# Kernel tuning notes

Measured on AMD Instinct MI355X. Metric: run time of the kernel, lower is better.

## Reference

```python
import jax, jax.numpy as jnp
import numpy as np

B, N, F, T = 8, 4096, 3, 12
D = 64            # model_dim
AH, DK, DV = 4, 32, 32   # attention headers, k_dim, v_dim
GH = 8            # gat_headers == out_features
E = 524288


def _ln(x, g, b, eps=1e-5):
    m = jnp.mean(x, -1, keepdims=True)
    v = jnp.mean((x - m) ** 2, -1, keepdims=True)
    return (x - m) * jax.lax.rsqrt(v + eps) * g + b


def _glu(x, w, b, C):
    # x: [B, C, N, L], w: [2C, C, 1, k] -> causal-style valid conv + SiLU gate
    y = jax.lax.conv_general_dilated(x, w, (1, 1), 'VALID',
                                     dimension_numbers=('NCHW', 'OIHW', 'NCHW'))
    y = y + b[None, :, None, None]
    return jax.nn.silu(y[:, :C]) * y[:, C:]


def setup_inputs():
    key = jax.random.key(0)
    ks = jax.random.split(key, 20)
    s = jnp.float32(0.02)
    return {
        'data': jax.random.normal(ks[0], (B, N, F, T), jnp.float32),
        'edges': jax.random.randint(ks[1], (2, E), 0, B * N),
        'embT_w': jax.random.normal(ks[2], (T, N)) * s,
        'embT_g': jnp.ones((N,)), 'embT_b': jnp.zeros((N,)),
        'wq': jax.random.normal(ks[3], (N, AH * DK)) * s,
        'wk': jax.random.normal(ks[4], (N, AH * DK)) * s,
        'wv': jax.random.normal(ks[5], (N, AH * DV)) * s,
        'wo': jax.random.normal(ks[6], (AH * DV, N)) * s,
        'tat_g': jnp.ones((N,)), 'tat_b': jnp.zeros((N,)),
        'mix_w': jax.random.normal(ks[7], (D, T, F)) * s,
        'mix_b': jnp.zeros((D,)),
        'embS_w': jax.random.normal(ks[8], (N, D)) * s,
        'embS_g': jnp.ones((D,)), 'embS_b': jnp.zeros((D,)),
        'gat_wl': jax.random.normal(ks[9], (D, GH * T)) * s,
        'gat_bl': jnp.zeros((GH * T,)),
        'gat_wr': jax.random.normal(ks[10], (D, GH * T)) * s,
        'gat_br': jnp.zeros((GH * T,)),
        'gat_att': jax.random.normal(ks[11], (GH, T)) * s,
        'gat_bias': jnp.zeros((GH * T,)),
        'g3_w': jax.random.normal(ks[12], (2 * GH, GH, 1, 3)) * s, 'g3_b': jnp.zeros((2 * GH,)),
        'g5_w': jax.random.normal(ks[13], (2 * GH, GH, 1, 5)) * s, 'g5_b': jnp.zeros((2 * GH,)),
        'g7_w': jax.random.normal(ks[14], (2 * GH, GH, 1, 7)) * s, 'g7_b': jnp.zeros((2 * GH,)),
        'fc_w': jax.random.normal(ks[15], (3 * T - 12, T)) * s, 'fc_b': jnp.zeros((T,)),
        'res_w': jax.random.normal(ks[16], (GH, F)) * s, 'res_b': jnp.zeros((GH,)),
        'ln_g': jnp.ones((GH,)), 'ln_b': jnp.zeros((GH,)),
    }


def reference(data, edges, embT_w, embT_g, embT_b, wq, wk, wv, wo, tat_g, tat_b,
              mix_w, mix_b, embS_w, embS_g, embS_b,
              gat_wl, gat_bl, gat_wr, gat_br, gat_att, gat_bias,
              g3_w, g3_b, g5_w, g5_b, g7_w, g7_b, fc_w, fc_b,
              res_w, res_b, ln_g, ln_b):
    # ---- EmbedT: [B,N,F,T] -> [B,F,T,N] plus learned temporal positional table
    x = data.transpose(0, 2, 3, 1) + embT_w[None, None]
    x = _ln(x, embT_g, embT_b)

    # ---- Temporal MHA over T (model_dim = N), dropout = identity in eval
    resid = x
    q = (x @ wq).reshape(B, F, T, AH, DK)
    k = (x @ wk).reshape(B, F, T, AH, DK)
    v = (x @ wv).reshape(B, F, T, AH, DV)
    scores = jnp.einsum('bfqhd,bfkhd->bfhqk', q, k) / jnp.sqrt(jnp.float32(DK))
    attn = jax.nn.softmax(scores, axis=-1)
    ctx = jnp.einsum('bfhqk,bfkhd->bfqhd', attn, v).reshape(B, F, T, AH * DV)
    x = _ln(ctx @ wo + resid, tat_g, tat_b)

    # ---- feature_temporal_mixer: Conv2d(T, D, (1, F)) on [B,T,N,F] -> [B,N,D]
    x = jnp.einsum('bftn,dtf->bnd', x, mix_w) + mix_b

    # ---- EmbedS
    x = _ln(x + embS_w[None], embS_g, embS_b)

    # ---- GATv2Conv over B*N nodes (add_self_loops=True, leaky slope 0.2)
    BN = B * N
    xf = x.reshape(BN, D)
    xl = (xf @ gat_wl + gat_bl).reshape(BN, GH, T)
    xr = (xf @ gat_wr + gat_br).reshape(BN, GH, T)
    loop = jnp.arange(BN)
    src = jnp.concatenate([edges[0], loop])
    dst = jnp.concatenate([edges[1], loop])
    feat = jax.nn.leaky_relu(xl[src] + xr[dst], 0.2)          # [E+BN, GH, T]
    e = jnp.einsum('eht,ht->eh', feat, gat_att)
    m = jax.ops.segment_max(e, dst, num_segments=BN)
    ex = jnp.exp(e - m[dst])
    ssum = jax.ops.segment_sum(ex, dst, num_segments=BN)
    alpha = ex / ssum[dst]
    out = jax.ops.segment_sum(xl[src] * alpha[:, :, None], dst, num_segments=BN)
    out = out.reshape(BN, GH * T) + gat_bias

    res_gate = out.reshape(B, N, GH, T).transpose(0, 2, 1, 3)  # [B,GH,N,T]

    # ---- gated convs (GLU) kernels 3/5/7 -> concat -> fc
    g = jnp.concatenate([_glu(res_gate, g3_w, g3_b, GH),
                         _glu(res_gate, g5_w, g5_b, GH),
                         _glu(res_gate, g7_w, g7_b, GH)], axis=-1)  # [B,GH,N,3T-12]
    x = jax.nn.relu(g @ fc_w + fc_b)   # features_num == 3 branch

    # ---- residual 1x1 conv over feature channels of raw data
    x_res = jnp.einsum('bfnt,of->bont', data.transpose(0, 2, 1, 3), res_w) \
            + res_b[None, :, None, None]
    x = jax.nn.relu(x_res + x)         # [B,GH,N,T]
    x = _ln(x.transpose(0, 3, 2, 1), ln_g, ln_b)  # LN over GH on [B,T,N,GH]
    return x.transpose(0, 2, 3, 1)     # [B,N,GH,T]
```

## Files before the change

kernel.cpp:

```cpp
#include <hip/hip_runtime.h>
#include <hip/hip_bf16.h>

typedef __hip_bfloat16 bf16;
typedef short bf16x8 __attribute__((ext_vector_type(8)));
typedef float f32x4 __attribute__((ext_vector_type(4)));
typedef unsigned short u16x4 __attribute__((ext_vector_type(4)));

constexpr int B = 8, N = 4096, F = 3, T = 12;
constexpr int Dm = 64, AH = 4, DK = 32;
constexpr int GH = 8;
constexpr int E = 524288;
constexpr int BN = B * N;
constexpr int ROWS = B * F * T;
constexpr int HD = AH * DK;
constexpr int PSZ = ROWS * 384;
constexpr int KSPLIT = 8;

__device__ __forceinline__ float b2f(bf16 x) { return __bfloat162float(x); }
__device__ __forceinline__ float u2f(unsigned short u) {
  return __uint_as_float(((unsigned)u) << 16);
}
__device__ __forceinline__ float ldf(const void* p, size_t i, int fl) {
  return fl ? b2f(((const bf16*)p)[i]) : ((const float*)p)[i];
}

constexpr unsigned C_EMBTW=0, C_EMBTG=49152, C_EMBTB=53248, C_WQ=57344,
  C_WK=581632, C_WV=1105920, C_WO=1630208, C_TATG=2154496, C_TATB=2158592,
  C_MIXW=2162688, C_MIXB=2164992, C_EMBSW=2165056, C_EMBSG=2427200,
  C_EMBSB=2427264, C_GWL=2427328, C_GBL=2433472, C_GWR=2433568,
  C_GBR=2439712, C_GATT=2439808, C_GBIAS=2439904, C_G3W=2440000,
  C_G3B=2440384, C_G5W=2440400, C_G5B=2441040, C_G7W=2441056,
  C_G7B=2441952, C_FCW=2441968, C_FCB=2442256, C_RW=2442268, C_RB=2442292,
  C_LNG=2442300, C_LNB=2442308, C_TOT=2442316;

__device__ const unsigned CUM[33] = {
  0,49152,53248,57344,581632,1105920,1630208,2154496,2158592,2162688,
  2164992,2165056,2427200,2427264,2427328,2433472,2433568,2439712,2439808,
  2439904,2440000,2440384,2440400,2441040,2441056,2441952,2441968,2442256,
  2442268,2442292,2442300,2442308,2442316};

constexpr size_t OFF_CVT = 16;
constexpr size_t OFF_X1  = OFF_CVT + 2442320;
constexpr size_t OFF_CTXB= OFF_X1  + (size_t)ROWS * N;
constexpr size_t OFF_X2  = OFF_CTXB+ (size_t)ROWS * HD;
constexpr size_t OFF_X3  = OFF_X2  + (size_t)ROWS * N;
constexpr size_t OFF_XL  = OFF_X3  + (size_t)BN * Dm;
constexpr size_t OFF_XR  = OFF_XL  + (size_t)BN * GH * T / 2;
constexpr size_t OFF_RG  = OFF_XR  + (size_t)BN * GH * T / 2;
constexpr size_t OFF_INT = OFF_RG  + (size_t)BN * GH * T;
constexpr size_t OFF_X2R = OFF_INT + 600000;
constexpr size_t OFF_WT16 = OFF_RG;
constexpr size_t OFF_X1B  = OFF_RG + 786432 + 262144;
constexpr size_t OFF_PP   = OFF_X1B + 294912;
constexpr size_t OFF_WOT  = OFF_PP + (size_t)KSPLIT * PSZ;
constexpr size_t OFF_GWT  = OFF_WOT + 262144;

struct Srcs { const void* p[32]; };

__global__ __launch_bounds__(256) void k_prep(
    const unsigned* __restrict__ g1, Srcs s, float* __restrict__ cv,
    int* __restrict__ cnt, bf16* __restrict__ wt, bf16* __restrict__ wot,
    bf16* __restrict__ wlrt) {
  __shared__ float tf[32][33];
  __shared__ bf16 tb[32][33];
  int fl = (g1[0] != 0x3F800000u);
  int blk = blockIdx.x;
  int tid = threadIdx.x;
  if (blk < 2048) {
    for (unsigned gid = blk * 256 + tid; gid < C_TOT + (unsigned)BN;
         gid += 2048 * 256) {
      if (gid < C_TOT) {
        int lo = 0, hi = 31;
        while (lo < hi) { int mid = (lo + hi + 1) >> 1; if (gid >= CUM[mid]) lo = mid; else hi = mid - 1; }
        if (lo >= 3 && lo <= 6) continue;
        unsigned off = gid - CUM[lo];
        cv[gid] = ldf(s.p[lo], off, fl);
      } else {
        cnt[gid - C_TOT] = 0;
      }
    }
  } else if (blk < 3584) {
    int bid = blk - 2048;
    int tc = bid / 128, tk = bid - tc * 128;
    int k0 = tk * 32, c0 = tc * 32;
    int mat = c0 >> 7, cloc = c0 & 127;
    const void* src = s.p[3 + mat];
    int r = tid >> 5, cc = tid & 31;
#pragma unroll
    for (int p = 0; p < 4; p++) {
      int row = p * 8 + r;
      tf[row][cc] = ldf(src, (size_t)(k0 + row) * 128 + cloc + cc, fl);
    }
    __syncthreads();
#pragma unroll
    for (int p = 0; p < 4; p++) {
      int crow = p * 8 + r;
      wt[(size_t)(c0 + crow) * 4096 + k0 + cc] = __float2bfloat16(tf[cc][crow]);
    }
  } else if (blk < 4096) {
    int bid = blk - 3584;
    int tn = bid >> 2, tk = bid & 3;
    int n0 = tn * 32, k0 = tk * 32;
    const void* wo = s.p[6];
    int r = tid >> 5, cc = tid & 31;
#pragma unroll
    for (int p = 0; p < 4; p++) {
      int row = p * 8 + r;
      size_t idx = (size_t)(k0 + row) * 4096 + n0 + cc;
      tb[row][cc] = fl ? ((const bf16*)wo)[idx]
                       : __float2bfloat16(((const float*)wo)[idx]);
    }
    __syncthreads();
#pragma unroll
    for (int p = 0; p < 4; p++) {
      int crow = p * 8 + r;
      wot[(size_t)(n0 + crow) * 128 + k0 + cc] = tb[cc][crow];
    }
  } else {
    int idx = (blk - 4096) * 256 + tid;
    if (idx < 192 * 64) {
      int c = idx >> 6, k = idx & 63;
      float v = (c < 96) ? ldf(s.p[14], (size_t)k * 96 + c, fl)
                         : ldf(s.p[16], (size_t)k * 96 + (c - 96), fl);
      wlrt[idx] = __float2bfloat16(v);
    }
  }
}

__global__ __launch_bounds__(1024) void k_embt_hist(
    const unsigned* __restrict__ g1, const void* __restrict__ data,
    const void* __restrict__ embw, const void* __restrict__ embg,
    const void* __restrict__ embb, float* __restrict__ x1,
    bf16* __restrict__ x1b, const int* __restrict__ edges,
    int* __restrict__ cnt) {
  __shared__ float red[32];
  int tid = threadIdx.x;
  int fl = (g1[0] != 0x3F800000u);
  if (blockIdx.x >= ROWS) {
    int e = (blockIdx.x - ROWS) * 1024 + tid;
    if (e < E) atomicAdd(cnt + edges[E + e], 1);
    return;
  }
  int row = blockIdx.x;
  int t = row % T; int bf_ = row / T; int f = bf_ % F; int bb = bf_ / F;
  float dv[4];
#pragma unroll
  for (int i = 0; i < 4; i++) {
    int n = i * 1024 + tid;
    dv[i] = ldf(data, (size_t)(bb * N + n) * 36 + f * 12 + t, fl);
  }
  float vals[4]; float s = 0.f, s2 = 0.f;
#pragma unroll
  for (int i = 0; i < 4; i++) {
    int n = i * 1024 + tid;
    float v = dv[i] + ldf(embw, (size_t)t * N + n, fl);
    vals[i] = v; s += v; s2 += v * v;
  }
#pragma unroll
  for (int o = 32; o > 0; o >>= 1) { s += __shfl_down(s, o, 64); s2 += __shfl_down(s2, o, 64); }
  int lane = tid & 63, wid = tid >> 6;
  if (lane == 0) { red[wid] = s; red[16 + wid] = s2; }
  __syncthreads();
  float S = 0.f, S2 = 0.f;
#pragma unroll
  for (int j = 0; j < 16; j++) { S += red[j]; S2 += red[16 + j]; }
  float mean = S / (float)N;
  float var = S2 / (float)N - mean * mean;
  float inv = rsqrtf(var + 1e-5f);
#pragma unroll
  for (int i = 0; i < 4; i++) {
    int n = i * 1024 + tid;
    float o = (vals[i] - mean) * inv * ldf(embg, n, fl) + ldf(embb, n, fl);
    x1[(size_t)row * N + n] = o;
    x1b[(size_t)row * N + n] = __float2bfloat16(o);
  }
}

__global__ __launch_bounds__(256) void k_qkv_scan(
    const bf16* __restrict__ x1b, const bf16* __restrict__ wt,
    float* __restrict__ pp, const int* __restrict__ cnt,
    int* __restrict__ off, int* __restrict__ cur) {
  __shared__ int part[256];
  int tid = threadIdx.x;
  if (blockIdx.x == 864) {
    int base = tid * 128;
    int s = 0;
    for (int j = 0; j < 128; j++) s += cnt[base + j];
    part[tid] = s;
    __syncthreads();
    for (int d = 1; d < 256; d <<= 1) {
      int v = (tid >= d) ? part[tid - d] : 0;
      __syncthreads();
      part[tid] += v;
      __syncthreads();
    }
    int run = part[tid] - s;
    for (int j = 0; j < 128; j++) {
      int c = cnt[base + j];
      off[base + j] = run; cur[base + j] = run;
      run += c;
    }
    if (tid == 255) off[BN] = E;
    return;
  }
  int wave = (blockIdx.x * 256 + tid) >> 6;
  int lane = tid & 63;
  int ks = wave & 7, tile = wave >> 3;
  int mt = tile / 24, nt = tile - mt * 24;
  int m = lane & 15, quad = lane >> 4;
  const bf16* ap = x1b + (size_t)(mt * 16 + m) * 4096 + ks * 512 + quad * 8;
  const bf16* bp = wt  + (size_t)(nt * 16 + m) * 4096 + ks * 512 + quad * 8;
  f32x4 acc = {0.f, 0.f, 0.f, 0.f};
  for (int kk = 0; kk < 512; kk += 32) {
    bf16x8 a = *(const bf16x8*)(ap + kk);
    bf16x8 b = *(const bf16x8*)(bp + kk);
    acc = __builtin_amdgcn_mfma_f32_16x16x32_bf16(a, b, acc, 0, 0, 0);
  }
  float* o = pp + ((size_t)ks * ROWS + mt * 16 + quad * 4) * 384 + nt * 16 + m;
#pragma unroll
  for (int r = 0; r < 4; r++) o[(size_t)r * 384] = acc[r];
}

__global__ __launch_bounds__(256) void k_attn_scatter(
    const float* __restrict__ pp, bf16* __restrict__ ctxb,
    const int* __restrict__ edges, int* __restrict__ cur,
    int* __restrict__ srcs) {
  if (blockIdx.x >= 24) {
    int e = (blockIdx.x - 24) * 256 + threadIdx.x;
    if (e < E) {
      int pos = atomicAdd(cur + edges[E + e], 1);
      srcs[pos] = edges[e];
    }
    return;
  }
  int bf_ = blockIdx.x;
  int h = threadIdx.x >> 6;
  int tid = threadIdx.x & 63;
  __shared__ float qs[4][12][32], ks[4][12][32], vs[4][12][32], att[4][12][12];
  for (int idx = tid; idx < 384; idx += 64) {
    int t = idx >> 5, d = idx & 31;
    int base = (bf_ * T + t) * 384 + h * 32 + d;
    float qv = 0.f, kv = 0.f, vv = 0.f;
#pragma unroll
    for (int p = 0; p < KSPLIT; p++) {
      qv += pp[(size_t)p * PSZ + base];
      kv += pp[(size_t)p * PSZ + base + 128];
      vv += pp[(size_t)p * PSZ + base + 256];
    }
    qs[h][t][d] = qv; ks[h][t][d] = kv; vs[h][t][d] = vv;
  }
  __syncthreads();
  for (int idx = tid; idx < 144; idx += 64) {
    int qt = idx / 12, kt = idx - qt * 12;
    float s = 0.f;
#pragma unroll
    for (int d = 0; d < 32; d++) s += qs[h][qt][d] * ks[h][kt][d];
    att[h][qt][kt] = s * 0.1767766953f;
  }
  __syncthreads();
  if (tid < 12) {
    float m = -1e30f;
#pragma unroll
    for (int j = 0; j < 12; j++) m = fmaxf(m, att[h][tid][j]);
    float ss = 0.f;
#pragma unroll
    for (int j = 0; j < 12; j++) { float e = __expf(att[h][tid][j] - m); att[h][tid][j] = e; ss += e; }
    float inv = 1.f / ss;
#pragma unroll
    for (int j = 0; j < 12; j++) att[h][tid][j] *= inv;
  }
  __syncthreads();
  for (int idx = tid; idx < 384; idx += 64) {
    int t = idx >> 5, d = idx & 31;
    float s = 0.f;
#pragma unroll
    for (int j = 0; j < 12; j++) s += att[h][t][j] * vs[h][j][d];
    ctxb[(size_t)(bf_ * T + t) * HD + h * 32 + d] = __float2bfloat16(s);
  }
}

__global__ __launch_bounds__(256) void k_proj_mma(
    const bf16* __restrict__ ctxb, const bf16* __restrict__ wot,
    const float* __restrict__ x1, float* __restrict__ x2r) {
  int wave = (blockIdx.x * 256 + threadIdx.x) >> 6;
  int lane = threadIdx.x & 63;
  int nt = wave & 255, mt = wave >> 8;
  int m = lane & 15, quad = lane >> 4;
  const bf16* ap = ctxb + (size_t)(mt * 16 + m) * 128 + quad * 8;
  const bf16* bp = wot  + (size_t)(nt * 16 + m) * 128 + quad * 8;
  f32x4 acc = {0.f, 0.f, 0.f, 0.f};
#pragma unroll
  for (int kk = 0; kk < 128; kk += 32) {
    bf16x8 a = *(const bf16x8*)(ap + kk);
    bf16x8 b = *(const bf16x8*)(bp + kk);
    acc = __builtin_amdgcn_mfma_f32_16x16x32_bf16(a, b, acc, 0, 0, 0);
  }
  int row0 = mt * 16 + quad * 4, col = nt * 16 + m;
#pragma unroll
  for (int r = 0; r < 4; r++) {
    size_t idx = (size_t)(row0 + r) * N + col;
    x2r[idx] = acc[r] + x1[idx];
  }
}

__global__ __launch_bounds__(1024) void k_ln2(
    const float* __restrict__ x2r, const float* __restrict__ g,
    const float* __restrict__ b_, float* __restrict__ x2) {
  __shared__ float red[32];
  int row = blockIdx.x, tid = threadIdx.x;
  float vals[4]; float s = 0.f, s2 = 0.f;
#pragma unroll
  for (int i = 0; i < 4; i++) {
    int n = i * 1024 + tid;
    float v = x2r[(size_t)row * N + n];
    vals[i] = v; s += v; s2 += v * v;
  }
#pragma unroll
  for (int o = 32; o > 0; o >>= 1) { s += __shfl_down(s, o, 64); s2 += __shfl_down(s2, o, 64); }
  int lane = tid & 63, wid = tid >> 6;
  if (lane == 0) { red[wid] = s; red[16 + wid] = s2; }
  __syncthreads();
  float S = 0.f, S2 = 0.f;
#pragma unroll
  for (int j = 0; j < 16; j++) { S += red[j]; S2 += red[16 + j]; }
  float mean = S / (float)N;
  float var = S2 / (float)N - mean * mean;
  float inv = rsqrtf(var + 1e-5f);
#pragma unroll
  for (int i = 0; i < 4; i++) {
    int n = i * 1024 + tid;
    x2[(size_t)row * N + n] = (vals[i] - mean) * inv * g[n] + b_[n];
  }
}

__global__ __launch_bounds__(256) void k_mix_ln(
    const float* __restrict__ x2, const float* __restrict__ mw,
    const float* __restrict__ mb, const float* __restrict__ sw,
    const float* __restrict__ g, const float* __restrict__ b_,
    bf16* __restrict__ x3b) {
  int tid = threadIdx.x; int wid = tid >> 6; int d = tid & 63;
  int ng = blockIdx.x * 4 + wid;
  int bb = ng >> 12; int n = ng & (N - 1);
  float acc = mb[d];
#pragma unroll
  for (int t = 0; t < T; t++)
#pragma unroll
    for (int f = 0; f < F; f++)
      acc += x2[((size_t)(bb * F + f) * T + t) * N + n] * mw[(d * T + t) * F + f];
  acc += sw[(size_t)n * Dm + d];
  float s = acc, s2 = acc * acc;
#pragma unroll
  for (int m = 1; m < 64; m <<= 1) { s += __shfl_xor(s, m, 64); s2 += __shfl_xor(s2, m, 64); }
  float mean = s * (1.f / 64.f), var = s2 * (1.f / 64.f) - mean * mean;
  float inv = rsqrtf(var + 1e-5f);
  x3b[(size_t)ng * Dm + d] = __float2bfloat16((acc - mean) * inv * g[d] + b_[d]);
}

__global__ __launch_bounds__(256) void k_gat_mma(
    const bf16* __restrict__ x3b, const bf16* __restrict__ wlrt,
    const float* __restrict__ bl, const float* __restrict__ br,
    bf16* __restrict__ xl, bf16* __restrict__ xr) {
  __shared__ __align__(16) bf16 bs[192 * 64];
  int tid = threadIdx.x;
  {
    const bf16x8* src = (const bf16x8*)wlrt;
    bf16x8* dst = (bf16x8*)bs;
#pragma unroll
    for (int i = 0; i < 6; i++) {
      int ci = i * 256 + tid;
      dst[ci ^ ((ci >> 3) & 7)] = src[ci];
    }
  }
  __syncthreads();
  int wave = tid >> 6, lane = tid & 63;
  int mt = blockIdx.x * 4 + wave;
  int m = lane & 15, quad = lane >> 4;
  const bf16* ap = x3b + (size_t)(mt * 16 + m) * 64 + quad * 8;
  bf16x8 a0 = *(const bf16x8*)(ap);
  bf16x8 a1 = *(const bf16x8*)(ap + 32);
  const bf16x8* bs8 = (const bf16x8*)bs;
  int row0 = mt * 16 + quad * 4;
#pragma unroll
  for (int nt = 0; nt < 12; nt++) {
    int r = nt * 16 + m;
    int c0 = r * 8 + quad;
    bf16x8 b0 = bs8[c0 ^ (r & 7)];
    bf16x8 b1 = bs8[(c0 + 4) ^ (r & 7)];
    f32x4 acc = {0.f, 0.f, 0.f, 0.f};
    acc = __builtin_amdgcn_mfma_f32_16x16x32_bf16(a0, b0, acc, 0, 0, 0);
    acc = __builtin_amdgcn_mfma_f32_16x16x32_bf16(a1, b1, acc, 0, 0, 0);
    bool left = r < 96;
    int c = left ? r : r - 96;
    float bias = left ? bl[c] : br[c];
    bf16* o = left ? xl : xr;
#pragma unroll
    for (int rr = 0; rr < 4; rr++)
      o[(size_t)(row0 + rr) * 96 + c] = __float2bfloat16(acc[rr] + bias);
  }
}

__device__ __forceinline__ void ld12bf(const bf16* p, float* l) {
  u16x4 a = *(const u16x4*)p;
  u16x4 b = *(const u16x4*)(p + 4);
  u16x4 c = *(const u16x4*)(p + 8);
  l[0]=u2f(a.x); l[1]=u2f(a.y); l[2]=u2f(a.z); l[3]=u2f(a.w);
  l[4]=u2f(b.x); l[5]=u2f(b.y); l[6]=u2f(b.z); l[7]=u2f(b.w);
  l[8]=u2f(c.x); l[9]=u2f(c.y); l[10]=u2f(c.z); l[11]=u2f(c.w);
}

__global__ __launch_bounds__(256) void k_gat(
    const int* __restrict__ off, const int* __restrict__ srcs,
    const bf16* __restrict__ xl, const bf16* __restrict__ xr,
    const float* __restrict__ att, const float* __restrict__ bias,
    float* __restrict__ rg) {
  int tid = threadIdx.x;
  int wv = tid >> 6, lane = tid & 63;
  int es = lane >> 3, h = lane & 7;
  int dst = blockIdx.x * 4 + wv;
  int bb = dst >> 12, n = dst & (N - 1);
  size_t rbase = (size_t)dst * 96 + h * 12;
  float xd[12], at[12];
  ld12bf(xr + rbase, xd);
#pragma unroll
  for (int t = 0; t < 12; t++) at[t] = att[h * 12 + t];

  float acc[12];
#pragma unroll
  for (int t = 0; t < 12; t++) acc[t] = 0.f;
  float ssum = 0.f;
  if (es == 0) {
    float l[12];
    ld12bf(xl + rbase, l);
    float sc = 0.f;
#pragma unroll
    for (int t = 0; t < 12; t++) {
      float sv = l[t] + xd[t];
      float fr = sv > 0.f ? sv : 0.2f * sv;
      sc += fr * at[t];
    }
    float ex = __expf(sc);
    ssum = ex;
#pragma unroll
    for (int t = 0; t < 12; t++) acc[t] = l[t] * ex;
  }
  int st = off[dst], en = off[dst + 1];
  for (int j = st + es; j < en; j += 8) {
    int src = srcs[j];
    float l[12];
    ld12bf(xl + (size_t)src * 96 + h * 12, l);
    float sc = 0.f;
#pragma unroll
    for (int t = 0; t < 12; t++) {
      float sv = l[t] + xd[t];
      float fr = sv > 0.f ? sv : 0.2f * sv;
      sc += fr * at[t];
    }
    float ex = __expf(sc);
    ssum += ex;
#pragma unroll
    for (int t = 0; t < 12; t++) acc[t] += l[t] * ex;
  }
#pragma unroll
  for (int m = 8; m < 64; m <<= 1) {
    ssum += __shfl_xor(ssum, m, 64);
#pragma unroll
    for (int t = 0; t < 12; t++) acc[t] += __shfl_xor(acc[t], m, 64);
  }
  if (es == 0) {
    float inv = 1.f / ssum;
    float* op = rg + ((size_t)(bb * 8 + h) * N + n) * 12;
#pragma unroll
    for (int t = 0; t < 12; t++)
      op[t] = acc[t] * inv + bias[h * 12 + t];
  }
}

__global__ __launch_bounds__(768) void k_tail(
    const unsigned* __restrict__ g1, const float* __restrict__ rg,
    const float* __restrict__ g3w, const float* __restrict__ g3b,
    const float* __restrict__ g5w, const float* __restrict__ g5b,
    const float* __restrict__ g7w, const float* __restrict__ g7b,
    const float* __restrict__ fcw, const float* __restrict__ fcb,
    const void* __restrict__ data, const float* __restrict__ rw,
    const float* __restrict__ rb, const float* __restrict__ lng,
    const float* __restrict__ lnb, void* __restrict__ out) {
  int tid = threadIdx.x;
  int br = tid >> 8;
  int u = tid & 255;
  int h = u & 7, i = u >> 3;
  int blk = blockIdx.x;
  int bb = blk >> 7;
  int n0 = (blk & 127) * 32;
  int n = n0 + i;
  int fl = (g1[0] != 0x3F800000u);
  __shared__ float xs[32][100];
  __shared__ float dds[32][40];
  __shared__ float wpk[8 * 260 + 4];
  __shared__ float fcs[288];
  __shared__ float gbuf[24][256];
  __shared__ float b3s[16], b5s[16], b7s[16], fcbs[12], lngs[8], lnbs[8], rws[24], rbs[8];
  for (int idx = tid; idx < 3072; idx += 768) {
    int c = idx / 384; int within = idx - c * 384;
    int ii = within / 12, t = within - ii * 12;
    xs[ii][c * 12 + t] = rg[((size_t)(bb * 8 + c) * N + n0 + ii) * 12 + t];
  }
  for (int idx = tid; idx < 1152; idx += 768) {
    int nn = idx / 36, jj = idx - nn * 36;
    dds[nn][jj] = ldf(data, (size_t)(bb * N + n0 + nn) * 36 + jj, fl);
  }
  for (int idx = tid; idx < 1920; idx += 768) {
    int hh = idx / 240; int r = idx - hh * 240; int c = r / 30; int tap = r - c * 30;
    float v;
    if (tap < 3)       v = g3w[hh * 24 + c * 3 + tap];
    else if (tap < 6)  v = g3w[(hh + 8) * 24 + c * 3 + (tap - 3)];
    else if (tap < 11) v = g5w[hh * 40 + c * 5 + (tap - 6)];
    else if (tap < 16) v = g5w[(hh + 8) * 40 + c * 5 + (tap - 11)];
    else if (tap < 23) v = g7w[hh * 56 + c * 7 + (tap - 16)];
    else               v = g7w[(hh + 8) * 56 + c * 7 + (tap - 23)];
    wpk[hh * 260 + c * 32 + tap] = v;
  }
  for (int idx = tid; idx < 288; idx += 768) fcs[idx] = fcw[idx];
  if (tid < 16) { b3s[tid] = g3b[tid]; b5s[tid] = g5b[tid]; b7s[tid] = g7b[tid]; }
  if (tid < 12) fcbs[tid] = fcb[tid];
  if (tid < 24) rws[tid] = rw[tid];
  if (tid < 8) { lngs[tid] = lng[tid]; lnbs[tid] = lnb[tid]; rbs[tid] = rb[tid]; }
  __syncthreads();
  const float* x = xs[i];
  const float* wbase = &wpk[h * 260];
  if (br == 0) {
    float pa[10], pb[10];
    float ba = b3s[h], bbv = b3s[h + 8];
#pragma unroll
    for (int l = 0; l < 10; l++) { pa[l] = ba; pb[l] = bbv; }
#pragma unroll
    for (int c = 0; c < 8; c++) {
      float4 xa = *(const float4*)&x[c * 12];
      float4 xb = *(const float4*)&x[c * 12 + 4];
      float4 xc = *(const float4*)&x[c * 12 + 8];
      float xr[12] = {xa.x, xa.y, xa.z, xa.w, xb.x, xb.y, xb.z, xb.w,
                      xc.x, xc.y, xc.z, xc.w};
      const float* wpc = wbase + c * 32;
      float4 wA = *(const float4*)wpc;
      float2 wB = *(const float2*)(wpc + 4);
#pragma unroll
      for (int l = 0; l < 10; l++) {
        pa[l] += xr[l] * wA.x + xr[l + 1] * wA.y + xr[l + 2] * wA.z;
        pb[l] += xr[l] * wA.w + xr[l + 1] * wB.x + xr[l + 2] * wB.y;
      }
    }
#pragma unroll
    for (int l = 0; l < 10; l++)
      gbuf[l][u] = pa[l] / (1.f + __expf(-pa[l])) * pb[l];
  } else if (br == 1) {
    float pa[8], pb[8];
    float ba = b5s[h], bbv = b5s[h + 8];
#pragma unroll
    for (int l = 0; l < 8; l++) { pa[l] = ba; pb[l] = bbv; }
#pragma unroll
    for (int c = 0; c < 8; c++) {
      float4 xa = *(const float4*)&x[c * 12];
      float4 xb = *(const float4*)&x[c * 12 + 4];
      float4 xc = *(const float4*)&x[c * 12 + 8];
      float xr[12] = {xa.x, xa.y, xa.z, xa.w, xb.x, xb.y, xb.z, xb.w,
                      xc.x, xc.y, xc.z, xc.w};
      const float* wpc = wbase + c * 32;
      float2 w0 = *(const float2*)(wpc + 6);
      float2 w1 = *(const float2*)(wpc + 8);
      float2 w2 = *(const float2*)(wpc + 10);
      float2 w3 = *(const float2*)(wpc + 12);
      float2 w4 = *(const float2*)(wpc + 14);
      float wt[10] = {w0.x, w0.y, w1.x, w1.y, w2.x, w2.y, w3.x, w3.y, w4.x, w4.y};
#pragma unroll
      for (int l = 0; l < 8; l++) {
        float a = 0.f, bsum = 0.f;
#pragma unroll
        for (int j = 0; j < 5; j++) { a += xr[l + j] * wt[j]; bsum += xr[l + j] * wt[5 + j]; }
        pa[l] += a; pb[l] += bsum;
      }
    }
#pragma unroll
    for (int l = 0; l < 8; l++)
      gbuf[10 + l][u] = pa[l] / (1.f + __expf(-pa[l])) * pb[l];
  } else {
    float pa[6], pb[6];
    float ba = b7s[h], bbv = b7s[h + 8];
#pragma unroll
    for (int l = 0; l < 6; l++) { pa[l] = ba; pb[l] = bbv; }
#pragma unroll
    for (int c = 0; c < 8; c++) {
      float4 xa = *(const float4*)&x[c * 12];
      float4 xb = *(const float4*)&x[c * 12 + 4];
      float4 xc = *(const float4*)&x[c * 12 + 8];
      float xr[12] = {xa.x, xa.y, xa.z, xa.w, xb.x, xb.y, xb.z, xb.w,
                      xc.x, xc.y, xc.z, xc.w};
      const float* wpc = wbase + c * 32;
      float4 wA = *(const float4*)(wpc + 16);
      float4 wB = *(const float4*)(wpc + 20);
      float4 wC = *(const float4*)(wpc + 24);
      float2 wD = *(const float2*)(wpc + 28);
      float wt[14] = {wA.x, wA.y, wA.z, wA.w, wB.x, wB.y, wB.z, wB.w,
                      wC.x, wC.y, wC.z, wC.w, wD.x, wD.y};
#pragma unroll
      for (int l = 0; l < 6; l++) {
        float a = 0.f, bsum = 0.f;
#pragma unroll
        for (int j = 0; j < 7; j++) { a += xr[l + j] * wt[j]; bsum += xr[l + j] * wt[7 + j]; }
        pa[l] += a; pb[l] += bsum;
      }
    }
#pragma unroll
    for (int l = 0; l < 6; l++)
      gbuf[18 + l][u] = pa[l] / (1.f + __expf(-pa[l])) * pb[l];
  }
  __syncthreads();
  if (br == 0) {
    float gv[24];
#pragma unroll
    for (int l = 0; l < 24; l++) gv[l] = gbuf[l][u];
    float rw0 = rws[h * 3 + 0], rw1 = rws[h * 3 + 1], rw2 = rws[h * 3 + 2], rb0 = rbs[h];
    size_t obase = ((size_t)(bb * N + n) * GH + h) * T;
#pragma unroll
    for (int t = 0; t < 12; t++) {
      float a = fcbs[t];
#pragma unroll
      for (int l = 0; l < 24; l++) a += gv[l] * fcs[l * 12 + t];
      a = fmaxf(a, 0.f);
      float r = rb0 + dds[i][t] * rw0 + dds[i][12 + t] * rw1 + dds[i][24 + t] * rw2;
      float v = fmaxf(a + r, 0.f);
      float s = v, s2 = v * v;
#pragma unroll
      for (int m = 1; m < 8; m <<= 1) { s += __shfl_xor(s, m, 64); s2 += __shfl_xor(s2, m, 64); }
      float mean = s * 0.125f, var = s2 * 0.125f - mean * mean;
      float inv = rsqrtf(var + 1e-5f);
      float o = (v - mean) * inv * lngs[h] + lnbs[h];
      if (fl) ((bf16*)out)[obase + t] = __float2bfloat16(o);
      else    ((float*)out)[obase + t] = o;
    }
  }
}

extern "C" void kernel_launch(void* const* d_in, const int* in_sizes, int n_in,
                              void* d_out, int out_size, void* d_ws, size_t ws_size,
                              hipStream_t stream) {
  const void* data  = d_in[0];
  const int*  edges = (const int*)d_in[1];
  const unsigned* g1 = (const unsigned*)d_in[3];

  float* ws = (float*)d_ws;
  float* cv  = ws + OFF_CVT;
  float* x1  = ws + OFF_X1;  float* x2 = ws + OFF_X2;
  float* x2r = ws + OFF_X2R;
  bf16* x3b  = (bf16*)(ws + OFF_X3);
  bf16* ctxb = (bf16*)(ws + OFF_CTXB);
  bf16* xl   = (bf16*)(ws + OFF_XL);
  bf16* xr   = (bf16*)(ws + OFF_XR);
  float* rg  = ws + OFF_RG;
  bf16* wt16 = (bf16*)(ws + OFF_WT16);
  bf16* x1b  = (bf16*)(ws + OFF_X1B);
  bf16* wot16= (bf16*)(ws + OFF_WOT);
  bf16* wlrt = (bf16*)(ws + OFF_GWT);
  float* pp  = ws + OFF_PP;
  int* ibase = (int*)(ws + OFF_INT);
  int* cnt  = ibase;
  int* off  = ibase + BN;
  int* srcs = ibase + 2 * BN + 16;

  Srcs s;
  for (int i = 0; i < 32; i++) s.p[i] = d_in[2 + i];

  k_prep<<<4144, 256, 0, stream>>>(g1, s, cv, cnt, wt16, wot16, wlrt);
  k_embt_hist<<<ROWS + 512, 1024, 0, stream>>>(g1, data, d_in[2], d_in[3],
                                               d_in[4], x1, x1b, edges, cnt);
  k_qkv_scan<<<865, 256, 0, stream>>>(x1b, wt16, pp, cnt, off, cnt);
  k_attn_scatter<<<24 + 2048, 256, 0, stream>>>(pp, ctxb, edges, cnt, srcs);
  k_proj_mma<<<1152, 256, 0, stream>>>(ctxb, wot16, x1, x2r);
  k_ln2<<<ROWS, 1024, 0, stream>>>(x2r, cv + C_TATG, cv + C_TATB, x2);
  k_mix_ln<<<BN / 4, 256, 0, stream>>>(x2, cv + C_MIXW, cv + C_MIXB, cv + C_EMBSW,
                                       cv + C_EMBSG, cv + C_EMBSB, x3b);
  k_gat_mma<<<512, 256, 0, stream>>>(x3b, wlrt, cv + C_GBL, cv + C_GBR, xl, xr);
  k_gat<<<BN / 4, 256, 0, stream>>>(off, srcs, xl, xr, cv + C_GATT, cv + C_GBIAS, rg);
  k_tail<<<BN / 32, 768, 0, stream>>>(g1, rg, cv + C_G3W, cv + C_G3B, cv + C_G5W,
                                      cv + C_G5B, cv + C_G7W, cv + C_G7B, cv + C_FCW,
                                      cv + C_FCB, data, cv + C_RW, cv + C_RB,
                                      cv + C_LNG, cv + C_LNB, d_out);
}
```

Measured before the change: 331.2 us.

## Fuse mix-LN into GAT projection and GAT aggregation into tail kernel

The mix+layernorm stage now writes its bf16 rows into shared memory inside the GAT projection MMA kernel, so the x3b global round trip goes away. The GAT edge aggregation moves into the tail kernel, which grows to 1024 threads and writes per-node results straight to shared memory instead of the rg buffer. This removes two launches and two intermediate global buffers. In exchange, the mix stage has lower parallelism (512 blocks, each wave looping over 16 rows) and the tail kernel uses larger blocks, which may lower occupancy; there is also a __syncthreads inside a divergent branch, with the idle threads calling a matching one.

```diff
diff --git a/kernel.cpp b/kernel.cpp
--- a/kernel.cpp
+++ b/kernel.cpp
@@ -333,34 +333,15 @@
   }
 }
 
-__global__ __launch_bounds__(256) void k_mix_ln(
+__global__ __launch_bounds__(256) void k_mix_gat(
     const float* __restrict__ x2, const float* __restrict__ mw,
     const float* __restrict__ mb, const float* __restrict__ sw,
     const float* __restrict__ g, const float* __restrict__ b_,
-    bf16* __restrict__ x3b) {
-  int tid = threadIdx.x; int wid = tid >> 6; int d = tid & 63;
-  int ng = blockIdx.x * 4 + wid;
-  int bb = ng >> 12; int n = ng & (N - 1);
-  float acc = mb[d];
-#pragma unroll
-  for (int t = 0; t < T; t++)
-#pragma unroll
-    for (int f = 0; f < F; f++)
-      acc += x2[((size_t)(bb * F + f) * T + t) * N + n] * mw[(d * T + t) * F + f];
-  acc += sw[(size_t)n * Dm + d];
-  float s = acc, s2 = acc * acc;
-#pragma unroll
-  for (int m = 1; m < 64; m <<= 1) { s += __shfl_xor(s, m, 64); s2 += __shfl_xor(s2, m, 64); }
-  float mean = s * (1.f / 64.f), var = s2 * (1.f / 64.f) - mean * mean;
-  float inv = rsqrtf(var + 1e-5f);
-  x3b[(size_t)ng * Dm + d] = __float2bfloat16((acc - mean) * inv * g[d] + b_[d]);
-}
-
-__global__ __launch_bounds__(256) void k_gat_mma(
-    const bf16* __restrict__ x3b, const bf16* __restrict__ wlrt,
-    const float* __restrict__ bl, const float* __restrict__ br,
-    bf16* __restrict__ xl, bf16* __restrict__ xr) {
+    const bf16* __restrict__ wlrt, const float* __restrict__ bl,
+    const float* __restrict__ br, bf16* __restrict__ xl,
+    bf16* __restrict__ xr) {
   __shared__ __align__(16) bf16 bs[192 * 64];
+  __shared__ __align__(16) bf16 x3s[64 * 64];
   int tid = threadIdx.x;
   {
     const bf16x8* src = (const bf16x8*)wlrt;
@@ -371,15 +352,39 @@
       dst[ci ^ ((ci >> 3) & 7)] = src[ci];
     }
   }
+  int wv = tid >> 6, lane = tid & 63;
+  int d = lane;
+  int row0 = blockIdx.x * 64;
+  float gd = g[d], bd = b_[d], mbd = mb[d];
+#pragma unroll 1
+  for (int rr = 0; rr < 16; rr++) {
+    int ng = row0 + wv * 16 + rr;
+    int bb = ng >> 12, n = ng & (N - 1);
+    float acc = mbd;
+#pragma unroll
+    for (int t = 0; t < T; t++)
+#pragma unroll
+      for (int f = 0; f < F; f++)
+        acc += x2[((size_t)(bb * F + f) * T + t) * N + n] * mw[(d * T + t) * F + f];
+    acc += sw[(size_t)n * Dm + d];
+    float s = acc, s2 = acc * acc;
+#pragma unroll
+    for (int m = 1; m < 64; m <<= 1) { s += __shfl_xor(s, m, 64); s2 += __shfl_xor(s2, m, 64); }
+    float mean = s * (1.f / 64.f), var = s2 * (1.f / 64.f) - mean * mean;
+    float inv = rsqrtf(var + 1e-5f);
+    float o = (acc - mean) * inv * gd + bd;
+    int r = wv * 16 + rr;
+    x3s[r * 64 + (((d >> 3) ^ (r & 7)) << 3) + (d & 7)] = __float2bfloat16(o);
+  }
   __syncthreads();
-  int wave = tid >> 6, lane = tid & 63;
-  int mt = blockIdx.x * 4 + wave;
   int m = lane & 15, quad = lane >> 4;
-  const bf16* ap = x3b + (size_t)(mt * 16 + m) * 64 + quad * 8;
-  bf16x8 a0 = *(const bf16x8*)(ap);
-  bf16x8 a1 = *(const bf16x8*)(ap + 32);
+  int lrow = wv * 16 + m;
+  const bf16x8* x3s8 = (const bf16x8*)x3s;
+  bf16x8 a0 = x3s8[lrow * 8 + (quad ^ (lrow & 7))];
+  bf16x8 a1 = x3s8[lrow * 8 + ((quad + 4) ^ (lrow & 7))];
   const bf16x8* bs8 = (const bf16x8*)bs;
-  int row0 = mt * 16 + quad * 4;
+  int mt = blockIdx.x * 4 + wv;
+  int orow0 = mt * 16 + quad * 4;
 #pragma unroll
   for (int nt = 0; nt < 12; nt++) {
     int r = nt * 16 + m;
@@ -395,7 +400,7 @@
     bf16* o = left ? xl : xr;
 #pragma unroll
     for (int rr = 0; rr < 4; rr++)
-      o[(size_t)(row0 + rr) * 96 + c] = __float2bfloat16(acc[rr] + bias);
+      o[(size_t)(orow0 + rr) * 96 + c] = __float2bfloat16(acc[rr] + bias);
   }
 }
 
@@ -408,75 +413,11 @@
   l[8]=u2f(c.x); l[9]=u2f(c.y); l[10]=u2f(c.z); l[11]=u2f(c.w);
 }
 
-__global__ __launch_bounds__(256) void k_gat(
-    const int* __restrict__ off, const int* __restrict__ srcs,
-    const bf16* __restrict__ xl, const bf16* __restrict__ xr,
-    const float* __restrict__ att, const float* __restrict__ bias,
-    float* __restrict__ rg) {
-  int tid = threadIdx.x;
-  int wv = tid >> 6, lane = tid & 63;
-  int es = lane >> 3, h = lane & 7;
-  int dst = blockIdx.x * 4 + wv;
-  int bb = dst >> 12, n = dst & (N - 1);
-  size_t rbase = (size_t)dst * 96 + h * 12;
-  float xd[12], at[12];
-  ld12bf(xr + rbase, xd);
-#pragma unroll
-  for (int t = 0; t < 12; t++) at[t] = att[h * 12 + t];
-
-  float acc[12];
-#pragma unroll
-  for (int t = 0; t < 12; t++) acc[t] = 0.f;
-  float ssum = 0.f;
-  if (es == 0) {
-    float l[12];
-    ld12bf(xl + rbase, l);
-    float sc = 0.f;
-#pragma unroll
-    for (int t = 0; t < 12; t++) {
-      float sv = l[t] + xd[t];
-      float fr = sv > 0.f ? sv : 0.2f * sv;
-      sc += fr * at[t];
-    }
-    float ex = __expf(sc);
-    ssum = ex;
-#pragma unroll
-    for (int t = 0; t < 12; t++) acc[t] = l[t] * ex;
-  }
-  int st = off[dst], en = off[dst + 1];
-  for (int j = st + es; j < en; j += 8) {
-    int src = srcs[j];
-    float l[12];
-    ld12bf(xl + (size_t)src * 96 + h * 12, l);
-    float sc = 0.f;
-#pragma unroll
-    for (int t = 0; t < 12; t++) {
-      float sv = l[t] + xd[t];
-      float fr = sv > 0.f ? sv : 0.2f * sv;
-      sc += fr * at[t];
-    }
-    float ex = __expf(sc);
-    ssum += ex;
-#pragma unroll
-    for (int t = 0; t < 12; t++) acc[t] += l[t] * ex;
-  }
-#pragma unroll
-  for (int m = 8; m < 64; m <<= 1) {
-    ssum += __shfl_xor(ssum, m, 64);
-#pragma unroll
-    for (int t = 0; t < 12; t++) acc[t] += __shfl_xor(acc[t], m, 64);
-  }
-  if (es == 0) {
-    float inv = 1.f / ssum;
-    float* op = rg + ((size_t)(bb * 8 + h) * N + n) * 12;
-#pragma unroll
-    for (int t = 0; t < 12; t++)
-      op[t] = acc[t] * inv + bias[h * 12 + t];
-  }
-}
-
-__global__ __launch_bounds__(768) void k_tail(
-    const unsigned* __restrict__ g1, const float* __restrict__ rg,
+__global__ __launch_bounds__(1024) void k_gat_tail(
+    const unsigned* __restrict__ g1, const int* __restrict__ off,
+    const int* __restrict__ srcs, const bf16* __restrict__ xl,
+    const bf16* __restrict__ xr, const float* __restrict__ att,
+    const float* __restrict__ gbias,
     const float* __restrict__ g3w, const float* __restrict__ g3b,
     const float* __restrict__ g5w, const float* __restrict__ g5b,
     const float* __restrict__ g7w, const float* __restrict__ g7b,
@@ -485,13 +426,9 @@
     const float* __restrict__ rb, const float* __restrict__ lng,
     const float* __restrict__ lnb, void* __restrict__ out) {
   int tid = threadIdx.x;
-  int br = tid >> 8;
-  int u = tid & 255;
-  int h = u & 7, i = u >> 3;
   int blk = blockIdx.x;
   int bb = blk >> 7;
   int n0 = (blk & 127) * 32;
-  int n = n0 + i;
   int fl = (g1[0] != 0x3F800000u);
   __shared__ float xs[32][100];
   __shared__ float dds[32][40];
@@ -499,16 +436,11 @@
   __shared__ float fcs[288];
   __shared__ float gbuf[24][256];
   __shared__ float b3s[16], b5s[16], b7s[16], fcbs[12], lngs[8], lnbs[8], rws[24], rbs[8];
-  for (int idx = tid; idx < 3072; idx += 768) {
-    int c = idx / 384; int within = idx - c * 384;
-    int ii = within / 12, t = within - ii * 12;
-    xs[ii][c * 12 + t] = rg[((size_t)(bb * 8 + c) * N + n0 + ii) * 12 + t];
-  }
-  for (int idx = tid; idx < 1152; idx += 768) {
+  for (int idx = tid; idx < 1152; idx += 1024) {
     int nn = idx / 36, jj = idx - nn * 36;
     dds[nn][jj] = ldf(data, (size_t)(bb * N + n0 + nn) * 36 + jj, fl);
   }
-  for (int idx = tid; idx < 1920; idx += 768) {
+  for (int idx = tid; idx < 1920; idx += 1024) {
     int hh = idx / 240; int r = idx - hh * 240; int c = r / 30; int tap = r - c * 30;
     float v;
     if (tap < 3)       v = g3w[hh * 24 + c * 3 + tap];
@@ -519,123 +451,190 @@
     else               v = g7w[(hh + 8) * 56 + c * 7 + (tap - 23)];
     wpk[hh * 260 + c * 32 + tap] = v;
   }
-  for (int idx = tid; idx < 288; idx += 768) fcs[idx] = fcw[idx];
+  for (int idx = tid; idx < 288; idx += 1024) fcs[idx] = fcw[idx];
   if (tid < 16) { b3s[tid] = g3b[tid]; b5s[tid] = g5b[tid]; b7s[tid] = g7b[tid]; }
   if (tid < 12) fcbs[tid] = fcb[tid];
   if (tid < 24) rws[tid] = rw[tid];
   if (tid < 8) { lngs[tid] = lng[tid]; lnbs[tid] = lnb[tid]; rbs[tid] = rb[tid]; }
+  {
+    int wv = tid >> 6, lane = tid & 63;
+    int half = lane >> 5, es = (lane >> 3) & 3, h = lane & 7;
+    int nl = wv * 2 + half;
+    int dst = bb * N + n0 + nl;
+    size_t rbase = (size_t)dst * 96 + h * 12;
+    float xd[12], at[12];
+    ld12bf(xr + rbase, xd);
+#pragma unroll
+    for (int t = 0; t < 12; t++) at[t] = att[h * 12 + t];
+    float acc[12];
+#pragma unroll
+    for (int t = 0; t < 12; t++) acc[t] = 0.f;
+    float ssum = 0.f;
+    if (es == 0) {
+      float l[12];
+      ld12bf(xl + rbase, l);
+      float sc = 0.f;
+#pragma unroll
+      for (int t = 0; t < 12; t++) {
+        float sv = l[t] + xd[t];
+        float fr = sv > 0.f ? sv : 0.2f * sv;
+        sc += fr * at[t];
+      }
+      float ex = __expf(sc);
+      ssum = ex;
+#pragma unroll
+      for (int t = 0; t < 12; t++) acc[t] = l[t] * ex;
+    }
+    int st = off[dst], en = off[dst + 1];
+    for (int j = st + es; j < en; j += 4) {
+      int src = srcs[j];
+      float l[12];
+      ld12bf(xl + (size_t)src * 96 + h * 12, l);
+      float sc = 0.f;
+#pragma unroll
+      for (int t = 0; t < 12; t++) {
+        float sv = l[t] + xd[t];
+        float fr = sv > 0.f ? sv : 0.2f * sv;
+        sc += fr * at[t];
+      }
+      float ex = __expf(sc);
+      ssum += ex;
+#pragma unroll
+      for (int t = 0; t < 12; t++) acc[t] += l[t] * ex;
+    }
+#pragma unroll
+    for (int m = 8; m < 32; m <<= 1) {
+      ssum += __shfl_xor(ssum, m, 64);
+#pragma unroll
+      for (int t = 0; t < 12; t++) acc[t] += __shfl_xor(acc[t], m, 64);
+    }
+    if (es == 0) {
+      float inv = 1.f / ssum;
+#pragma unroll
+      for (int t = 0; t < 12; t++)
+        xs[nl][h * 12 + t] = acc[t] * inv + gbias[h * 12 + t];
+    }
+  }
   __syncthreads();
-  const float* x = xs[i];
-  const float* wbase = &wpk[h * 260];
-  if (br == 0) {
-    float pa[10], pb[10];
-    float ba = b3s[h], bbv = b3s[h + 8];
-#pragma unroll
-    for (int l = 0; l < 10; l++) { pa[l] = ba; pb[l] = bbv; }
-#pragma unroll
-    for (int c = 0; c < 8; c++) {
-      float4 xa = *(const float4*)&x[c * 12];
-      float4 xb = *(const float4*)&x[c * 12 + 4];
-      float4 xc = *(const float4*)&x[c * 12 + 8];
-      float xr[12] = {xa.x, xa.y, xa.z, xa.w, xb.x, xb.y, xb.z, xb.w,
-                      xc.x, xc.y, xc.z, xc.w};
-      const float* wpc = wbase + c * 32;
-      float4 wA = *(const float4*)wpc;
-      float2 wB = *(const float2*)(wpc + 4);
-#pragma unroll
-      for (int l = 0; l < 10; l++) {
-        pa[l] += xr[l] * wA.x + xr[l + 1] * wA.y + xr[l + 2] * wA.z;
-        pb[l] += xr[l] * wA.w + xr[l + 1] * wB.x + xr[l + 2] * wB.y;
+  if (tid < 768) {
+    int br = tid >> 8;
+    int u = tid & 255;
+    int h = u & 7, i = u >> 3;
+    int n = n0 + i;
+    const float* x = xs[i];
+    const float* wbase = &wpk[h * 260];
+    if (br == 0) {
+      float pa[10], pb[10];
+      float ba = b3s[h], bbv = b3s[h + 8];
+#pragma unroll
+      for (int l = 0; l < 10; l++) { pa[l] = ba; pb[l] = bbv; }
+#pragma unroll
+      for (int c = 0; c < 8; c++) {
+        float4 xa = *(const float4*)&x[c * 12];
+        float4 xb = *(const float4*)&x[c * 12 + 4];
+        float4 xc = *(const float4*)&x[c * 12 + 8];
+        float xr_[12] = {xa.x, xa.y, xa.z, xa.w, xb.x, xb.y, xb.z, xb.w,
+                         xc.x, xc.y, xc.z, xc.w};
+        const float* wpc = wbase + c * 32;
+        float4 wA = *(const float4*)wpc;
+        float2 wB = *(const float2*)(wpc + 4);
+#pragma unroll
+        for (int l = 0; l < 10; l++) {
+          pa[l] += xr_[l] * wA.x + xr_[l + 1] * wA.y + xr_[l + 2] * wA.z;
+          pb[l] += xr_[l] * wA.w + xr_[l + 1] * wB.x + xr_[l + 2] * wB.y;
+        }
       }
-    }
-#pragma unroll
-    for (int l = 0; l < 10; l++)
-      gbuf[l][u] = pa[l] / (1.f + __expf(-pa[l])) * pb[l];
-  } else if (br == 1) {
-    float pa[8], pb[8];
-    float ba = b5s[h], bbv = b5s[h + 8];
-#pragma unroll
-    for (int l = 0; l < 8; l++) { pa[l] = ba; pb[l] = bbv; }
-#pragma unroll
-    for (int c = 0; c < 8; c++) {
-      float4 xa = *(const float4*)&x[c * 12];
-      float4 xb = *(const float4*)&x[c * 12 + 4];
-      float4 xc = *(const float4*)&x[c * 12 + 8];
-      float xr[12] = {xa.x, xa.y, xa.z, xa.w, xb.x, xb.y, xb.z, xb.w,
-                      xc.x, xc.y, xc.z, xc.w};
-      const float* wpc = wbase + c * 32;
-      float2 w0 = *(const float2*)(wpc + 6);
-      float2 w1 = *(const float2*)(wpc + 8);
-      float2 w2 = *(const float2*)(wpc + 10);
-      float2 w3 = *(const float2*)(wpc + 12);
-      float2 w4 = *(const float2*)(wpc + 14);
-      float wt[10] = {w0.x, w0.y, w1.x, w1.y, w2.x, w2.y, w3.x, w3.y, w4.x, w4.y};
-#pragma unroll
-      for (int l = 0; l < 8; l++) {
-        float a = 0.f, bsum = 0.f;
-#pragma unroll
-        for (int j = 0; j < 5; j++) { a += xr[l + j] * wt[j]; bsum += xr[l + j] * wt[5 + j]; }
-        pa[l] += a; pb[l] += bsum;
+#pragma unroll
+      for (int l = 0; l < 10; l++)
+        gbuf[l][u] = pa[l] / (1.f + __expf(-pa[l])) * pb[l];
+    } else if (br == 1) {
+      float pa[8], pb[8];
+      float ba = b5s[h], bbv = b5s[h + 8];
+#pragma unroll
+      for (int l = 0; l < 8; l++) { pa[l] = ba; pb[l] = bbv; }
+#pragma unroll
+      for (int c = 0; c < 8; c++) {
+        float4 xa = *(const float4*)&x[c * 12];
+        float4 xb = *(const float4*)&x[c * 12 + 4];
+        float4 xc = *(const float4*)&x[c * 12 + 8];
+        float xr_[12] = {xa.x, xa.y, xa.z, xa.w, xb.x, xb.y, xb.z, xb.w,
+                         xc.x, xc.y, xc.z, xc.w};
+        const float* wpc = wbase + c * 32;
+        float2 w0 = *(const float2*)(wpc + 6);
+        float2 w1 = *(const float2*)(wpc + 8);
+        float2 w2 = *(const float2*)(wpc + 10);
+        float2 w3 = *(const float2*)(wpc + 12);
+        float2 w4 = *(const float2*)(wpc + 14);
+        float wt[10] = {w0.x, w0.y, w1.x, w1.y, w2.x, w2.y, w3.x, w3.y, w4.x, w4.y};
+#pragma unroll
+        for (int l = 0; l < 8; l++) {
+          float a = 0.f, bsum = 0.f;
+#pragma unroll
+          for (int j = 0; j < 5; j++) { a += xr_[l + j] * wt[j]; bsum += xr_[l + j] * wt[5 + j]; }
+          pa[l] += a; pb[l] += bsum;
+        }
       }
-    }
-#pragma unroll
-    for (int l = 0; l < 8; l++)
-      gbuf[10 + l][u] = pa[l] / (1.f + __expf(-pa[l])) * pb[l];
+#pragma unroll
+      for (int l = 0; l < 8; l++)
+        gbuf[10 + l][u] = pa[l] / (1.f + __expf(-pa[l])) * pb[l];
+    } else {
+      float pa[6], pb[6];
+      float ba = b7s[h], bbv = b7s[h + 8];
+#pragma unroll
+      for (int l = 0; l < 6; l++) { pa[l] = ba; pb[l] = bbv; }
+#pragma unroll
+      for (int c = 0; c < 8; c++) {
+        float4 xa = *(const float4*)&x[c * 12];
+        float4 xb = *(const float4*)&x[c * 12 + 4];
+        float4 xc = *(const float4*)&x[c * 12 + 8];
+        float xr_[12] = {xa.x, xa.y, xa.z, xa.w, xb.x, xb.y, xb.z, xb.w,
+                         xc.x, xc.y, xc.z, xc.w};
+        const float* wpc = wbase + c * 32;
+        float4 wA = *(const float4*)(wpc + 16);
+        float4 wB = *(const float4*)(wpc + 20);
+        float4 wC = *(const float4*)(wpc + 24);
+        float2 wD = *(const float2*)(wpc + 28);
+        float wt[14] = {wA.x, wA.y, wA.z, wA.w, wB.x, wB.y, wB.z, wB.w,
+                        wC.x, wC.y, wC.z, wC.w, wD.x, wD.y};
+#pragma unroll
+        for (int l = 0; l < 6; l++) {
+          float a = 0.f, bsum = 0.f;
+#pragma unroll
+          for (int j = 0; j < 7; j++) { a += xr_[l + j] * wt[j]; bsum += xr_[l + j] * wt[7 + j]; }
+          pa[l] += a; pb[l] += bsum;
+        }
+      }
+#pragma unroll
+      for (int l = 0; l < 6; l++)
+        gbuf[18 + l][u] = pa[l] / (1.f + __expf(-pa[l])) * pb[l];
+    }
+    __syncthreads();
+    if (br == 0) {
+      float gv[24];
+#pragma unroll
+      for (int l = 0; l < 24; l++) gv[l] = gbuf[l][u];
+      float rw0 = rws[h * 3 + 0], rw1 = rws[h * 3 + 1], rw2 = rws[h * 3 + 2], rb0 = rbs[h];
+      size_t obase = ((size_t)(bb * N + n) * GH + h) * T;
+#pragma unroll
+      for (int t = 0; t < 12; t++) {
+        float a = fcbs[t];
+#pragma unroll
+        for (int l = 0; l < 24; l++) a += gv[l] * fcs[l * 12 + t];
+        a = fmaxf(a, 0.f);
+        float r = rb0 + dds[i][t] * rw0 + dds[i][12 + t] * rw1 + dds[i][24 + t] * rw2;
+        float v = fmaxf(a + r, 0.f);
+        float s = v, s2 = v * v;
+#pragma unroll
+        for (int m = 1; m < 8; m <<= 1) { s += __shfl_xor(s, m, 64); s2 += __shfl_xor(s2, m, 64); }
+        float mean = s * 0.125f, var = s2 * 0.125f - mean * mean;
+        float inv = rsqrtf(var + 1e-5f);
+        float o = (v - mean) * inv * lngs[h] + lnbs[h];
+        if (fl) ((bf16*)out)[obase + t] = __float2bfloat16(o);
+        else    ((float*)out)[obase + t] = o;
+      }
+    }
   } else {
-    float pa[6], pb[6];
-    float ba = b7s[h], bbv = b7s[h + 8];
-#pragma unroll
-    for (int l = 0; l < 6; l++) { pa[l] = ba; pb[l] = bbv; }
-#pragma unroll
-    for (int c = 0; c < 8; c++) {
-      float4 xa = *(const float4*)&x[c * 12];
-      float4 xb = *(const float4*)&x[c * 12 + 4];
-      float4 xc = *(const float4*)&x[c * 12 + 8];
-      float xr[12] = {xa.x, xa.y, xa.z, xa.w, xb.x, xb.y, xb.z, xb.w,
-                      xc.x, xc.y, xc.z, xc.w};
-      const float* wpc = wbase + c * 32;
-      float4 wA = *(const float4*)(wpc + 16);
-      float4 wB = *(const float4*)(wpc + 20);
-      float4 wC = *(const float4*)(wpc + 24);
-      float2 wD = *(const float2*)(wpc + 28);
-      float wt[14] = {wA.x, wA.y, wA.z, wA.w, wB.x, wB.y, wB.z, wB.w,
-                      wC.x, wC.y, wC.z, wC.w, wD.x, wD.y};
-#pragma unroll
-      for (int l = 0; l < 6; l++) {
-        float a = 0.f, bsum = 0.f;
-#pragma unroll
-        for (int j = 0; j < 7; j++) { a += xr[l + j] * wt[j]; bsum += xr[l + j] * wt[7 + j]; }
-        pa[l] += a; pb[l] += bsum;
-      }
-    }
-#pragma unroll
-    for (int l = 0; l < 6; l++)
-      gbuf[18 + l][u] = pa[l] / (1.f + __expf(-pa[l])) * pb[l];
-  }
-  __syncthreads();
-  if (br == 0) {
-    float gv[24];
-#pragma unroll
-    for (int l = 0; l < 24; l++) gv[l] = gbuf[l][u];
-    float rw0 = rws[h * 3 + 0], rw1 = rws[h * 3 + 1], rw2 = rws[h * 3 + 2], rb0 = rbs[h];
-    size_t obase = ((size_t)(bb * N + n) * GH + h) * T;
-#pragma unroll
-    for (int t = 0; t < 12; t++) {
-      float a = fcbs[t];
-#pragma unroll
-      for (int l = 0; l < 24; l++) a += gv[l] * fcs[l * 12 + t];
-      a = fmaxf(a, 0.f);
-      float r = rb0 + dds[i][t] * rw0 + dds[i][12 + t] * rw1 + dds[i][24 + t] * rw2;
-      float v = fmaxf(a + r, 0.f);
-      float s = v, s2 = v * v;
-#pragma unroll
-      for (int m = 1; m < 8; m <<= 1) { s += __shfl_xor(s, m, 64); s2 += __shfl_xor(s2, m, 64); }
-      float mean = s * 0.125f, var = s2 * 0.125f - mean * mean;
-      float inv = rsqrtf(var + 1e-5f);
-      float o = (v - mean) * inv * lngs[h] + lnbs[h];
-      if (fl) ((bf16*)out)[obase + t] = __float2bfloat16(o);
-      else    ((float*)out)[obase + t] = o;
-    }
+    __syncthreads();
   }
 }
 
@@ -650,11 +649,9 @@
   float* cv  = ws + OFF_CVT;
   float* x1  = ws + OFF_X1;  float* x2 = ws + OFF_X2;
   float* x2r = ws + OFF_X2R;
-  bf16* x3b  = (bf16*)(ws + OFF_X3);
   bf16* ctxb = (bf16*)(ws + OFF_CTXB);
   bf16* xl   = (bf16*)(ws + OFF_XL);
   bf16* xr   = (bf16*)(ws + OFF_XR);
-  float* rg  = ws + OFF_RG;
   bf16* wt16 = (bf16*)(ws + OFF_WT16);
   bf16* x1b  = (bf16*)(ws + OFF_X1B);
   bf16* wot16= (bf16*)(ws + OFF_WOT);
@@ -675,12 +672,13 @@
   k_attn_scatter<<<24 + 2048, 256, 0, stream>>>(pp, ctxb, edges, cnt, srcs);
   k_proj_mma<<<1152, 256, 0, stream>>>(ctxb, wot16, x1, x2r);
   k_ln2<<<ROWS, 1024, 0, stream>>>(x2r, cv + C_TATG, cv + C_TATB, x2);
-  k_mix_ln<<<BN / 4, 256, 0, stream>>>(x2, cv + C_MIXW, cv + C_MIXB, cv + C_EMBSW,
-                                       cv + C_EMBSG, cv + C_EMBSB, x3b);
-  k_gat_mma<<<512, 256, 0, stream>>>(x3b, wlrt, cv + C_GBL, cv + C_GBR, xl, xr);
-  k_gat<<<BN / 4, 256, 0, stream>>>(off, srcs, xl, xr, cv + C_GATT, cv + C_GBIAS, rg);
-  k_tail<<<BN / 32, 768, 0, stream>>>(g1, rg, cv + C_G3W, cv + C_G3B, cv + C_G5W,
-                                      cv + C_G5B, cv + C_G7W, cv + C_G7B, cv + C_FCW,
-                                      cv + C_FCB, data, cv + C_RW, cv + C_RB,
-                                      cv + C_LNG, cv + C_LNB, d_out);
-}
+  k_mix_gat<<<512, 256, 0, stream>>>(x2, cv + C_MIXW, cv + C_MIXB, cv + C_EMBSW,
+                                     cv + C_EMBSG, cv + C_EMBSB, wlrt,
+                                     cv + C_GBL, cv + C_GBR, xl, xr);
+  k_gat_tail<<<BN / 32, 1024, 0, stream>>>(g1, off, srcs, xl, xr, cv + C_GATT,
+                                           cv + C_GBIAS, cv + C_G3W, cv + C_G3B,
+                                           cv + C_G5W, cv + C_G5B, cv + C_G7W,
+                                           cv + C_G7B, cv + C_FCW, cv + C_FCB,
+                                           data, cv + C_RW, cv + C_RB,
+                                           cv + C_LNG, cv + C_LNB, d_out);
+}
```

After: 319.1 us. 3.7% less time.
